# Kernel tuning notes

Measured on AMD Instinct MI355X. Metric: run time of the kernel, lower is better.

The kernel has to match this reference:

```python
import jax, jax.numpy as jnp
import numpy as np

BP_ITERS = 7  # CRF(num_ways, 7)
EPS = 1e-6


def _row_norm(A):
    return A / (A.sum(-1, keepdims=True) + EPS)


def _clamp_supports(belief, onehot, num_supports):
    # support nodes (first num_supports) have observed labels -> clamp beliefs
    is_sup = (jnp.arange(belief.shape[1]) < num_supports)[None, :, None]
    return jnp.where(is_sup, onehot, belief)


def _loopy_bp(unary, binary, A, onehot, num_supports):
    # iterative CRF mean-field / loopy belief propagation over affinity graph
    log_u = jax.nn.log_softmax(unary, axis=-1)                 # [B,N,W]
    b0 = _clamp_supports(jax.nn.softmax(unary, axis=-1), onehot, num_supports)
    def step(b, _):
        # message: aggregate neighbor beliefs through pairwise compatibility
        msg = jnp.einsum('bij,bjw,bwv->biv', A, b, binary)     # [B,N,W]
        b = jax.nn.softmax(log_u + msg, axis=-1)
        return _clamp_supports(b, onehot, num_supports), None
    belief, _ = jax.lax.scan(step, b0, None, length=BP_ITERS)
    return belief


def _aff_update(bp_aff, belief):
    # refined affinity = base affinity modulated by belief agreement, row-normed
    sim = jnp.einsum('biw,bjw->bij', belief, belief)
    return _row_norm(bp_aff * sim)


def _gcn(X, A, W, b):
    return jax.nn.relu(jnp.einsum('bij,bjd,de->bie', _row_norm(A), X, W) + b)


def _binary_comp_calc(X, onehot):
    # class prototypes from labeled nodes -> pairwise label compatibility
    counts = onehot.sum(1)                                      # [B,W]
    proto = jnp.einsum('bnw,bnd->bwd', onehot, X) / (counts[..., None] + EPS)
    proto = proto / (jnp.linalg.norm(proto, axis=-1, keepdims=True) + EPS)
    return jax.nn.softmax(jnp.einsum('bwd,bvd->bwv', proto, proto), axis=-1)


def setup_inputs() -> dict:
    B, N, D, W, S = 128, 512, 128, 5, 256
    key = jax.random.key(0)
    ks = jax.random.split(key, 12)
    inp = {}
    inp['inp_data'] = jax.random.normal(ks[0], (B, N, D), jnp.float32)
    inp['affinity_mat'] = jax.random.uniform(ks[1], (B, N, N), jnp.float32)
    inp['unary_comp'] = jax.random.normal(ks[2], (B, N, W), jnp.float32)
    inp['binary_comp'] = jax.random.normal(ks[3], (B, W, W), jnp.float32)
    inp['all_label'] = jax.random.randint(ks[4], (B, N), 0, W)
    inp['all_data'] = jax.random.normal(ks[5], (B, N, D), jnp.float32)
    dims = [(128, 64), (64, 32), (32, 16)]
    for i, (di, do) in enumerate(dims):
        inp[f'W{i+1}'] = jax.random.normal(ks[6 + i], (di, do), jnp.float32) / np.sqrt(di)
        inp[f'b{i+1}'] = jnp.zeros((do,), jnp.float32)
    inp['batch_size'] = B
    inp['x_dim'] = N
    inp['y_dim'] = W
    inp['num_supports'] = S
    return inp


def reference(inp_data, affinity_mat, unary_comp, binary_comp, all_label, all_data,
              W1, b1, W2, b2, W3, b3, batch_size, x_dim, y_dim, num_supports):
    nw = unary_comp.shape[-1]
    onehot = jax.nn.one_hot(all_label, nw, dtype=inp_data.dtype)  # [B,N,W]
    A = affinity_mat
    # --- round 1: CRF BP with provided binary compat, then GCN 128->64 ---
    belief1 = _loopy_bp(unary_comp, binary_comp, A, onehot, num_supports)
    aff1 = _aff_update(A, belief1)
    X = _gcn(inp_data, A, W1, b1)
    bc = _binary_comp_calc(X, onehot)
    # --- round 2: GCN 64->32 ---
    belief2 = _loopy_bp(unary_comp, bc, A, onehot, num_supports)
    aff2 = _aff_update(A, belief2)
    X = _gcn(X, A, W2, b2)
    bc = _binary_comp_calc(X, onehot)
    # --- round 3: GCN 32->16 ---
    belief3 = _loopy_bp(unary_comp, bc, A, onehot, num_supports)
    aff3 = _aff_update(A, belief3)
    X = _gcn(X, A, W3, b3)
    return (A, (belief1, belief2, belief3), (aff1, aff2, aff3))
```

## Files before the change

kernel.cpp:

```cpp
#include <hip/hip_runtime.h>
#include <math.h>

#define EPSF 1e-6f
#define BP_ITERS 7

#define OFF_A    0ull
#define OFF_B1   33554432ull
#define OFF_B2   33882112ull
#define OFF_B3   34209792ull
#define OFF_AF1  34537472ull
#define OFF_AF2  68091904ull
#define OFF_AF3  101646336ull
#define Y1_OFF  (OFF_AF1)
#define X1_OFF  (OFF_AF1 + 4194304ull)
#define Y2_OFF  (OFF_AF2)
#define X2_OFF  (OFF_AF2 + 2097152ull)
#define AT_OFF  (OFF_AF2 + 4194304ull)
#define PARKB   (OFF_AF2 + 20971520ull)
#define RS_OFF  (OFF_AF3)

typedef __attribute__((ext_vector_type(8))) short bf16x8;
typedef __attribute__((ext_vector_type(4))) short s16x4;
typedef __attribute__((ext_vector_type(4))) float f32x4;

__device__ __forceinline__ short f2bf(float f) {
  unsigned u = __float_as_uint(f);
  unsigned r = (u + 0x7fffu + ((u >> 16) & 1u)) >> 16;
  return (short)r;
}
__device__ __forceinline__ float bf2f(short h) {
  return __uint_as_float(((unsigned)(unsigned short)h) << 16);
}

__global__ __launch_bounds__(256) void k_rowsum(const float* __restrict__ A, float* __restrict__ rs) {
  int wid = threadIdx.x >> 6, lane = threadIdx.x & 63;
  for (int rr = 0; rr < 2; ++rr) {
    size_t row = (size_t)blockIdx.x * 8 + wid * 2 + rr;
    const float4* src = (const float4*)(A + row * 512);
    float4 v0 = src[lane * 2], v1 = src[lane * 2 + 1];
    float s = v0.x + v0.y + v0.z + v0.w + v1.x + v1.y + v1.z + v1.w;
    #pragma unroll
    for (int off = 1; off < 64; off <<= 1) s += __shfl_xor(s, off, 64);
    if (lane == 0) rs[row] = s;
  }
}

template<int BN, bool POST>
__global__ __launch_bounds__(256) void k_mgemm(const float* __restrict__ Ain, size_t astride,
                                               const float* __restrict__ Bin, size_t bstride,
                                               float* __restrict__ Cout,
                                               const float* __restrict__ rowsum,
                                               const float* __restrict__ bias, int K) {
  constexpr int BM = 128, BK = 64, LDA = BK + 8;
  constexpr int NF = BN / 16;
  __shared__ short Ahi[BM * LDA], Alo[BM * LDA];
  __shared__ short Bhi[BN * LDA], Blo[BN * LDA];
  __shared__ float rs[BM];
  __shared__ float bls[BN];
  int b = blockIdx.x >> 2, mt = blockIdx.x & 3;
  int m0 = mt * BM;
  int t = threadIdx.x;
  int w = t >> 6, l = t & 63;
  if constexpr (POST) {
    if (t < BM) rs[t] = rowsum[(size_t)b * 512 + m0 + t];
    if (t < BN) bls[t] = bias[t];
  }
  const float* Ab = Ain + (size_t)b * astride + (size_t)m0 * K;
  const float* Bb = Bin + (size_t)b * bstride;
  f32x4 acc[2][NF];
  #pragma unroll
  for (int mf = 0; mf < 2; ++mf)
    #pragma unroll
    for (int nf = 0; nf < NF; ++nf) acc[mf][nf] = (f32x4){0.f, 0.f, 0.f, 0.f};

  for (int kt = 0; kt < K; kt += BK) {
    #pragma unroll
    for (int i = 0; i < 8; ++i) {
      int f = (t + i * 256) * 4;
      int r = f >> 6, k = f & 63;
      float4 v = *(const float4*)(Ab + (size_t)r * K + kt + k);
      float xs[4] = {v.x, v.y, v.z, v.w};
      s16x4 h, lo;
      #pragma unroll
      for (int e = 0; e < 4; ++e) {
        h[e] = f2bf(xs[e]);
        lo[e] = f2bf(xs[e] - bf2f(h[e]));
      }
      *(s16x4*)&Ahi[r * LDA + k] = h;
      *(s16x4*)&Alo[r * LDA + k] = lo;
    }
    #pragma unroll
    for (int i = 0; i < BK * BN / 1024; ++i) {
      int f = (t + i * 256) * 4;
      int k = f / BN, n = f % BN;
      float4 v = *(const float4*)(Bb + (size_t)(kt + k) * BN + n);
      float xs[4] = {v.x, v.y, v.z, v.w};
      #pragma unroll
      for (int e = 0; e < 4; ++e) {
        short h = f2bf(xs[e]);
        Bhi[(n + e) * LDA + k] = h;
        Blo[(n + e) * LDA + k] = f2bf(xs[e] - bf2f(h));
      }
    }
    __syncthreads();
    #pragma unroll
    for (int kc = 0; kc < 2; ++kc) {
      int kb = kc * 32 + (l >> 4) * 8;
      bf16x8 ah[2], al[2];
      #pragma unroll
      for (int mf = 0; mf < 2; ++mf) {
        int row = w * 32 + mf * 16 + (l & 15);
        ah[mf] = *(const bf16x8*)&Ahi[row * LDA + kb];
        al[mf] = *(const bf16x8*)&Alo[row * LDA + kb];
      }
      #pragma unroll
      for (int nf = 0; nf < NF; ++nf) {
        int col = nf * 16 + (l & 15);
        bf16x8 bh = *(const bf16x8*)&Bhi[col * LDA + kb];
        bf16x8 bl = *(const bf16x8*)&Blo[col * LDA + kb];
        #pragma unroll
        for (int mf = 0; mf < 2; ++mf) {
          acc[mf][nf] = __builtin_amdgcn_mfma_f32_16x16x32_bf16(ah[mf], bh, acc[mf][nf], 0, 0, 0);
          acc[mf][nf] = __builtin_amdgcn_mfma_f32_16x16x32_bf16(ah[mf], bl, acc[mf][nf], 0, 0, 0);
          acc[mf][nf] = __builtin_amdgcn_mfma_f32_16x16x32_bf16(al[mf], bh, acc[mf][nf], 0, 0, 0);
        }
      }
    }
    __syncthreads();
  }
  #pragma unroll
  for (int mf = 0; mf < 2; ++mf) {
    #pragma unroll
    for (int nf = 0; nf < NF; ++nf) {
      int col = nf * 16 + (l & 15);
      #pragma unroll
      for (int i = 0; i < 4; ++i) {
        int rloc = w * 32 + mf * 16 + (l >> 4) * 4 + i;
        float x = acc[mf][nf][i];
        if constexpr (POST) x = fmaxf(x / (rs[rloc] + EPSF) + bls[col], 0.f);
        Cout[((size_t)b * 512 + m0 + rloc) * BN + col] = x;
      }
    }
  }
}

template<int D>
__global__ __launch_bounds__(256) void k_bc(const float* __restrict__ X, const int* __restrict__ labels,
                                            float* __restrict__ dst, int parkoff) {
  constexpr int SL = 256 / D;
  constexpr int NPER = 512 / SL;
  __shared__ int labs[512];
  __shared__ float part[SL * 5 * D];
  __shared__ float cnt[5], nrm[5], proto[5 * D], dots[25];
  int b = blockIdx.x, t = threadIdx.x;
  labs[t] = labels[b * 512 + t];
  labs[t + 256] = labels[b * 512 + 256 + t];
  if (t < 5) { cnt[t] = 0.f; nrm[t] = 0.f; }
  __syncthreads();
  if (t < 128) {
    #pragma unroll
    for (int k = 0; k < 4; ++k) atomicAdd(&cnt[labs[t * 4 + k]], 1.f);
  }
  {
    int s = t / D, d = t % D;
    float a5[5] = {};
    for (int k = 0; k < NPER; ++k) {
      int n = s * NPER + k;
      float x = X[((size_t)b * 512 + n) * D + d];
      int lab = labs[n];
      #pragma unroll
      for (int w = 0; w < 5; ++w) a5[w] += (lab == w) ? x : 0.f;
    }
    #pragma unroll
    for (int w = 0; w < 5; ++w) part[(s * 5 + w) * D + d] = a5[w];
  }
  __syncthreads();
  for (int idx = t; idx < 5 * D; idx += 256) {
    int w = idx / D, dd = idx % D;
    float p = 0.f;
    #pragma unroll
    for (int s2 = 0; s2 < SL; ++s2) p += part[(s2 * 5 + w) * D + dd];
    p /= (cnt[w] + EPSF);
    proto[w * D + dd] = p;
    atomicAdd(&nrm[w], p * p);
  }
  __syncthreads();
  if (t < 25) {
    int w = t / 5, v = t % 5;
    float sdot = 0.f;
    for (int dd = 0; dd < D; ++dd) sdot += proto[w * D + dd] * proto[v * D + dd];
    dots[t] = sdot / ((sqrtf(nrm[w]) + EPSF) * (sqrtf(nrm[v]) + EPSF));
  }
  __syncthreads();
  if (t < 25) {
    int w = t / 5;
    float m = dots[w * 5];
    #pragma unroll
    for (int u = 1; u < 5; ++u) m = fmaxf(m, dots[w * 5 + u]);
    float ssum = 0.f;
    #pragma unroll
    for (int u = 0; u < 5; ++u) ssum += expf(dots[w * 5 + u] - m);
    dst[(size_t)b * 64 + parkoff + t] = expf(dots[t] - m) / ssum;
  }
}

__global__ __launch_bounds__(256) void k_At(const float* __restrict__ A, float* __restrict__ Atr) {
  __shared__ float T[64][65];
  int bid = blockIdx.x;
  int b = bid >> 5, r = bid & 31, jt = r >> 2, it = r & 3;
  int j0 = jt * 64, i0 = it * 64;
  int t = threadIdx.x;
  #pragma unroll
  for (int c = 0; c < 4; ++c) {
    int flat = (t + c * 256) * 4;
    int ii = flat >> 6, jj = flat & 63;
    float4 v = *(const float4*)(A + ((size_t)b * 512 + 256 + i0 + ii) * 512 + j0 + jj);
    T[ii][jj] = v.x; T[ii][jj + 1] = v.y; T[ii][jj + 2] = v.z; T[ii][jj + 3] = v.w;
  }
  __syncthreads();
  #pragma unroll
  for (int c = 0; c < 4; ++c) {
    int flat = (t + c * 256) * 4;
    int jj = flat >> 6, ii = flat & 63;
    float4 v = make_float4(T[ii][jj], T[ii + 1][jj], T[ii + 2][jj], T[ii + 3][jj]);
    *(float4*)(Atr + ((size_t)b * 512 + j0 + jj) * 256 + i0 + ii) = v;
  }
}

__global__ __launch_bounds__(1024, 4) void k_bp(const float* __restrict__ Atr,
                                                const float* __restrict__ unary,
                                                const float* __restrict__ binc,
                                                const int* __restrict__ labels,
                                                float* __restrict__ out) {
  __shared__ float cbuf[256 * 8];
  __shared__ float b3s[256 * 5];
  __shared__ float msg[256 * 5];
  __shared__ float binl[5 * 8];
  __shared__ int labs[256];
  int bid = blockIdx.x;
  int r = bid % 3, b = bid / 3;
  int t = threadIdx.x;
  int w = t >> 6, l = t & 63;
  int wh = w & 1, jc = w >> 1;
  int i0 = wh * 128 + l;
  if (t < 256) labs[t] = labels[b * 512 + t];
  if (t < 25) {
    float val;
    if (r == 0)      val = binc[b * 25 + t];
    else if (r == 1) val = out[PARKB + (size_t)b * 64 + t];
    else             val = out[PARKB + (size_t)b * 64 + 32 + t];
    binl[(t / 5) * 8 + (t % 5)] = val;
  }
  __syncthreads();
  float u[5] = {};
  if (t < 256) {
    size_t ub = ((size_t)b * 512 + 256 + t) * 5;
    #pragma unroll
    for (int v = 0; v < 5; ++v) u[v] = unary[ub + v];
    float m = u[0];
    #pragma unroll
    for (int v = 1; v < 5; ++v) m = fmaxf(m, u[v]);
    float e[5], ssum = 0.f;
    #pragma unroll
    for (int v = 0; v < 5; ++v) { e[v] = expf(u[v] - m); ssum += e[v]; }
    float inv = 1.f / ssum;
    #pragma unroll
    for (int v = 0; v < 5; ++v) b3s[t * 5 + v] = e[v] * inv;
    int lab = labs[t];
    #pragma unroll
    for (int v = 0; v < 5; ++v) cbuf[t * 8 + v] = binl[lab * 8 + v];
  }
  __syncthreads();
  float asup[2][5] = {};
  float af[32][2];
  #pragma unroll
  for (int jj = 0; jj < 32; ++jj) {
    int j = jc * 32 + jj;
    float4 cq = *(const float4*)&cbuf[j * 8];
    float c4 = cbuf[j * 8 + 4];
    float ck[5] = {cq.x, cq.y, cq.z, cq.w, c4};
    size_t sbase = ((size_t)b * 512 + j) * 256 + i0;
    float a0 = Atr[sbase], a1 = Atr[sbase + 64];
    #pragma unroll
    for (int k = 0; k < 5; ++k) { asup[0][k] += a0 * ck[k]; asup[1][k] += a1 * ck[k]; }
    size_t fbase = ((size_t)b * 512 + 256 + j) * 256 + i0;
    af[jj][0] = Atr[fbase]; af[jj][1] = Atr[fbase + 64];
  }
  __syncthreads();
  for (int it = 0; it < BP_ITERS; ++it) {
    if (t < 256) {
      float bb[5];
      #pragma unroll
      for (int v = 0; v < 5; ++v) bb[v] = b3s[t * 5 + v];
      #pragma unroll
      for (int v = 0; v < 5; ++v) {
        float s = 0.f;
        #pragma unroll
        for (int ww = 0; ww < 5; ++ww) s += bb[ww] * binl[ww * 8 + v];
        cbuf[t * 8 + v] = s;
      }
    }
    if (t < 1280) msg[t] = 0.f;
    if (t < 256) msg[t + 1024] = 0.f;
    __syncthreads();
    {
      float acc[2][5];
      #pragma unroll
      for (int g = 0; g < 2; ++g)
        #pragma unroll
        for (int k = 0; k < 5; ++k) acc[g][k] = asup[g][k];
      #pragma unroll
      for (int jj = 0; jj < 32; ++jj) {
        int j = jc * 32 + jj;
        float4 cq = *(const float4*)&cbuf[j * 8];
        float c4 = cbuf[j * 8 + 4];
        float ck[5] = {cq.x, cq.y, cq.z, cq.w, c4};
        #pragma unroll
        for (int k = 0; k < 5; ++k) {
          acc[0][k] += af[jj][0] * ck[k];
          acc[1][k] += af[jj][1] * ck[k];
        }
      }
      #pragma unroll
      for (int g = 0; g < 2; ++g)
        #pragma unroll
        for (int k = 0; k < 5; ++k) atomicAdd(&msg[(i0 + 64 * g) * 5 + k], acc[g][k]);
    }
    __syncthreads();
    if (t < 256) {
      float lg[5];
      #pragma unroll
      for (int v = 0; v < 5; ++v) lg[v] = u[v] + msg[t * 5 + v];
      float m = lg[0];
      #pragma unroll
      for (int v = 1; v < 5; ++v) m = fmaxf(m, lg[v]);
      float e[5], ssum = 0.f;
      #pragma unroll
      for (int v = 0; v < 5; ++v) { e[v] = expf(lg[v] - m); ssum += e[v]; }
      float inv = 1.f / ssum;
      #pragma unroll
      for (int v = 0; v < 5; ++v) b3s[t * 5 + v] = e[v] * inv;
    }
    __syncthreads();
  }
  if (t < 512) {
    int n = t;
    float bel[5];
    if (n < 256) {
      int lab = labs[n];
      #pragma unroll
      for (int v = 0; v < 5; ++v) bel[v] = (v == lab) ? 1.f : 0.f;
    } else {
      #pragma unroll
      for (int v = 0; v < 5; ++v) bel[v] = b3s[(n - 256) * 5 + v];
    }
    size_t base = OFF_B1 + (size_t)r * 327680ull + ((size_t)b * 512 + n) * 5;
    #pragma unroll
    for (int v = 0; v < 5; ++v) out[base + v] = bel[v];
  }
}

__global__ __launch_bounds__(256) void k_aff(const float* __restrict__ A, float* __restrict__ out) {
  __shared__ float belT[16][520];
  int bid = blockIdx.x;
  int b = bid >> 5, tile = bid & 31;
  int r0 = tile * 16;
  int t = threadIdx.x, w = t >> 6, l = t & 63;
  for (int idx = t; idx < 2560; idx += 256) {
    int j = idx / 5, v = idx % 5;
    belT[v][j]      = out[OFF_B1 + (size_t)b * 2560 + idx];
    belT[5 + v][j]  = out[OFF_B2 + (size_t)b * 2560 + idx];
    belT[10 + v][j] = out[OFF_B3 + (size_t)b * 2560 + idx];
  }
  __syncthreads();
  #pragma unroll 1
  for (int rr = 0; rr < 4; ++rr) {
    int row = r0 + w * 4 + rr;
    size_t base = ((size_t)b * 512 + row) * 512;
    float bi[15];
    #pragma unroll
    for (int k = 0; k < 15; ++k) bi[k] = belT[k][row];
    float a[8], s1[8], s2[8], s3[8];
    float p1 = 0.f, p2 = 0.f, p3 = 0.f;
    #pragma unroll
    for (int c = 0; c < 8; ++c) {
      int col = l + 64 * c;
      a[c] = A[base + col];
      float t1 = 0.f, t2 = 0.f, t3 = 0.f;
      #pragma unroll
      for (int v = 0; v < 5; ++v) {
        t1 += bi[v] * belT[v][col];
        t2 += bi[5 + v] * belT[5 + v][col];
        t3 += bi[10 + v] * belT[10 + v][col];
      }
      s1[c] = t1; s2[c] = t2; s3[c] = t3;
      p1 += a[c] * t1; p2 += a[c] * t2; p3 += a[c] * t3;
    }
    #pragma unroll
    for (int off = 1; off < 64; off <<= 1) {
      p1 += __shfl_xor(p1, off, 64);
      p2 += __shfl_xor(p2, off, 64);
      p3 += __shfl_xor(p3, off, 64);
    }
    float inv1 = 1.f / (p1 + EPSF), inv2 = 1.f / (p2 + EPSF), inv3 = 1.f / (p3 + EPSF);
    #pragma unroll
    for (int c = 0; c < 8; ++c) {
      int col = l + 64 * c;
      out[OFF_A   + base + col] = a[c];
      out[OFF_AF1 + base + col] = a[c] * s1[c] * inv1;
      out[OFF_AF2 + base + col] = a[c] * s2[c] * inv2;
      out[OFF_AF3 + base + col] = a[c] * s3[c] * inv3;
    }
  }
}

extern "C" void kernel_launch(void* const* d_in, const int* in_sizes, int n_in,
                              void* d_out, int out_size, void* d_ws, size_t ws_size,
                              hipStream_t stream) {
  (void)in_sizes; (void)n_in; (void)out_size; (void)d_ws; (void)ws_size;
  const float* inp  = (const float*)d_in[0];
  const float* aff  = (const float*)d_in[1];
  const float* una  = (const float*)d_in[2];
  const float* binc = (const float*)d_in[3];
  const int*   lab  = (const int*)d_in[4];
  const float* W1 = (const float*)d_in[6];
  const float* b1 = (const float*)d_in[7];
  const float* W2 = (const float*)d_in[8];
  const float* b2 = (const float*)d_in[9];
  float* out = (float*)d_out;

  k_rowsum<<<8192, 256, 0, stream>>>(aff, out + RS_OFF);
  k_mgemm<64, false><<<512, 256, 0, stream>>>(inp, 65536, W1, 0, out + Y1_OFF, nullptr, nullptr, 128);
  k_mgemm<64, true ><<<512, 256, 0, stream>>>(aff, 262144, out + Y1_OFF, 32768, out + X1_OFF, out + RS_OFF, b1, 512);
  k_bc<64><<<128, 256, 0, stream>>>(out + X1_OFF, lab, out + PARKB, 0);
  k_mgemm<32, false><<<512, 256, 0, stream>>>(out + X1_OFF, 32768, W2, 0, out + Y2_OFF, nullptr, nullptr, 64);
  k_mgemm<32, true ><<<512, 256, 0, stream>>>(aff, 262144, out + Y2_OFF, 16384, out + X2_OFF, out + RS_OFF, b2, 512);
  k_bc<32><<<128, 256, 0, stream>>>(out + X2_OFF, lab, out + PARKB, 32);
  k_At<<<4096, 256, 0, stream>>>(aff, out + AT_OFF);
  k_bp<<<384, 1024, 0, stream>>>(out + AT_OFF, una, binc, lab, out);
  k_aff<<<4096, 256, 0, stream>>>(aff, out);
}
```

Baseline: 591.9 us.

## Fuse affinity row sums into GEMM loads and vectorize affinity update kernel

Drops the separate row-sum kernel. The GCN aggregation GEMM now accumulates row sums of A through shared-memory atomics as it loads each A tile, which saves one full 128MB pass over the affinity matrix. The final affinity-update kernel now uses float4 loads and stores for A, the belief tables and the four outputs. The per-element shared atomics add contention inside the GEMM load loop, and the msg zeroing loses its guard, so with 1024 threads every thread now writes it.

Result: slower. 656.4 us (+10.9%).

```diff
diff --git a/kernel.cpp b/kernel.cpp
--- a/kernel.cpp
+++ b/kernel.cpp
@@ -17,7 +17,6 @@
 #define X2_OFF  (OFF_AF2 + 2097152ull)
 #define AT_OFF  (OFF_AF2 + 4194304ull)
 #define PARKB   (OFF_AF2 + 20971520ull)
-#define RS_OFF  (OFF_AF3)
 
 typedef __attribute__((ext_vector_type(8))) short bf16x8;
 typedef __attribute__((ext_vector_type(4))) short s16x4;
@@ -32,24 +31,10 @@
   return __uint_as_float(((unsigned)(unsigned short)h) << 16);
 }
 
-__global__ __launch_bounds__(256) void k_rowsum(const float* __restrict__ A, float* __restrict__ rs) {
-  int wid = threadIdx.x >> 6, lane = threadIdx.x & 63;
-  for (int rr = 0; rr < 2; ++rr) {
-    size_t row = (size_t)blockIdx.x * 8 + wid * 2 + rr;
-    const float4* src = (const float4*)(A + row * 512);
-    float4 v0 = src[lane * 2], v1 = src[lane * 2 + 1];
-    float s = v0.x + v0.y + v0.z + v0.w + v1.x + v1.y + v1.z + v1.w;
-    #pragma unroll
-    for (int off = 1; off < 64; off <<= 1) s += __shfl_xor(s, off, 64);
-    if (lane == 0) rs[row] = s;
-  }
-}
-
 template<int BN, bool POST>
 __global__ __launch_bounds__(256) void k_mgemm(const float* __restrict__ Ain, size_t astride,
                                                const float* __restrict__ Bin, size_t bstride,
                                                float* __restrict__ Cout,
-                                               const float* __restrict__ rowsum,
                                                const float* __restrict__ bias, int K) {
   constexpr int BM = 128, BK = 64, LDA = BK + 8;
   constexpr int NF = BN / 16;
@@ -62,8 +47,9 @@
   int t = threadIdx.x;
   int w = t >> 6, l = t & 63;
   if constexpr (POST) {
-    if (t < BM) rs[t] = rowsum[(size_t)b * 512 + m0 + t];
+    if (t < BM) rs[t] = 0.f;
     if (t < BN) bls[t] = bias[t];
+    __syncthreads();
   }
   const float* Ab = Ain + (size_t)b * astride + (size_t)m0 * K;
   const float* Bb = Bin + (size_t)b * bstride;
@@ -79,6 +65,7 @@
       int f = (t + i * 256) * 4;
       int r = f >> 6, k = f & 63;
       float4 v = *(const float4*)(Ab + (size_t)r * K + kt + k);
+      if constexpr (POST) atomicAdd(&rs[r], v.x + v.y + v.z + v.w);
       float xs[4] = {v.x, v.y, v.z, v.w};
       s16x4 h, lo;
       #pragma unroll
@@ -300,7 +287,7 @@
         cbuf[t * 8 + v] = s;
       }
     }
-    if (t < 1280) msg[t] = 0.f;
+    msg[t] = 0.f;
     if (t < 256) msg[t + 1024] = 0.f;
     __syncthreads();
     {
@@ -380,21 +367,29 @@
     float bi[15];
     #pragma unroll
     for (int k = 0; k < 15; ++k) bi[k] = belT[k][row];
-    float a[8], s1[8], s2[8], s3[8];
+    float4 a[2];
+    float s1[2][4], s2[2][4], s3[2][4];
     float p1 = 0.f, p2 = 0.f, p3 = 0.f;
     #pragma unroll
-    for (int c = 0; c < 8; ++c) {
-      int col = l + 64 * c;
-      a[c] = A[base + col];
-      float t1 = 0.f, t2 = 0.f, t3 = 0.f;
-      #pragma unroll
-      for (int v = 0; v < 5; ++v) {
-        t1 += bi[v] * belT[v][col];
-        t2 += bi[5 + v] * belT[5 + v][col];
-        t3 += bi[10 + v] * belT[10 + v][col];
-      }
-      s1[c] = t1; s2[c] = t2; s3[c] = t3;
-      p1 += a[c] * t1; p2 += a[c] * t2; p3 += a[c] * t3;
+    for (int g = 0; g < 2; ++g) {
+      int c0 = g * 256 + l * 4;
+      a[g] = *(const float4*)(A + base + c0);
+      float4 bv[15];
+      #pragma unroll
+      for (int k = 0; k < 15; ++k) bv[k] = *(const float4*)&belT[k][c0];
+      #pragma unroll
+      for (int e = 0; e < 4; ++e) {
+        float ae = ((const float*)&a[g])[e];
+        float t1 = 0.f, t2 = 0.f, t3 = 0.f;
+        #pragma unroll
+        for (int v = 0; v < 5; ++v) {
+          t1 += bi[v]      * ((const float*)&bv[v])[e];
+          t2 += bi[5 + v]  * ((const float*)&bv[5 + v])[e];
+          t3 += bi[10 + v] * ((const float*)&bv[10 + v])[e];
+        }
+        s1[g][e] = t1; s2[g][e] = t2; s3[g][e] = t3;
+        p1 += ae * t1; p2 += ae * t2; p3 += ae * t3;
+      }
     }
     #pragma unroll
     for (int off = 1; off < 64; off <<= 1) {
@@ -404,12 +399,20 @@
     }
     float inv1 = 1.f / (p1 + EPSF), inv2 = 1.f / (p2 + EPSF), inv3 = 1.f / (p3 + EPSF);
     #pragma unroll
-    for (int c = 0; c < 8; ++c) {
-      int col = l + 64 * c;
-      out[OFF_A   + base + col] = a[c];
-      out[OFF_AF1 + base + col] = a[c] * s1[c] * inv1;
-      out[OFF_AF2 + base + col] = a[c] * s2[c] * inv2;
-      out[OFF_AF3 + base + col] = a[c] * s3[c] * inv3;
+    for (int g = 0; g < 2; ++g) {
+      int c0 = g * 256 + l * 4;
+      float4 o1, o2, o3;
+      #pragma unroll
+      for (int e = 0; e < 4; ++e) {
+        float ae = ((const float*)&a[g])[e];
+        ((float*)&o1)[e] = ae * s1[g][e] * inv1;
+        ((float*)&o2)[e] = ae * s2[g][e] * inv2;
+        ((float*)&o3)[e] = ae * s3[g][e] * inv3;
+      }
+      *(float4*)(out + OFF_A   + base + c0) = a[g];
+      *(float4*)(out + OFF_AF1 + base + c0) = o1;
+      *(float4*)(out + OFF_AF2 + base + c0) = o2;
+      *(float4*)(out + OFF_AF3 + base + c0) = o3;
     }
   }
 }
@@ -429,12 +432,11 @@
   const float* b2 = (const float*)d_in[9];
   float* out = (float*)d_out;
 
-  k_rowsum<<<8192, 256, 0, stream>>>(aff, out + RS_OFF);
-  k_mgemm<64, false><<<512, 256, 0, stream>>>(inp, 65536, W1, 0, out + Y1_OFF, nullptr, nullptr, 128);
-  k_mgemm<64, true ><<<512, 256, 0, stream>>>(aff, 262144, out + Y1_OFF, 32768, out + X1_OFF, out + RS_OFF, b1, 512);
+  k_mgemm<64, false><<<512, 256, 0, stream>>>(inp, 65536, W1, 0, out + Y1_OFF, nullptr, 128);
+  k_mgemm<64, true ><<<512, 256, 0, stream>>>(aff, 262144, out + Y1_OFF, 32768, out + X1_OFF, b1, 512);
   k_bc<64><<<128, 256, 0, stream>>>(out + X1_OFF, lab, out + PARKB, 0);
-  k_mgemm<32, false><<<512, 256, 0, stream>>>(out + X1_OFF, 32768, W2, 0, out + Y2_OFF, nullptr, nullptr, 64);
-  k_mgemm<32, true ><<<512, 256, 0, stream>>>(aff, 262144, out + Y2_OFF, 16384, out + X2_OFF, out + RS_OFF, b2, 512);
+  k_mgemm<32, false><<<512, 256, 0, stream>>>(out + X1_OFF, 32768, W2, 0, out + Y2_OFF, nullptr, 64);
+  k_mgemm<32, true ><<<512, 256, 0, stream>>>(aff, 262144, out + Y2_OFF, 16384, out + X2_OFF, b2, 512);
   k_bc<32><<<128, 256, 0, stream>>>(out + X2_OFF, lab, out + PARKB, 32);
   k_At<<<4096, 256, 0, stream>>>(aff, out + AT_OFF);
   k_bp<<<384, 1024, 0, stream>>>(out + AT_OFF, una, binc, lab, out);
```
